# Performance work log

Hardware: AMD Instinct MI355X
Metric: run time of the kernel (lower is better)

## Reference

```python
import jax, jax.numpy as jnp
import numpy as np

_J6 = jnp.array([[0,0,0,0,0,1],[0,0,0,0,-1,0],[0,0,0,1,0,0],[0,0,1,0,0,0],[0,-1,0,0,0,0],[1,0,0,0,0,0]], dtype=jnp.float32)
# pairs (i,j) from combinations(range(4),2)
_PI = jnp.array([0,0,0,1,1,2])
_PJ = jnp.array([1,2,3,2,3,3])

def exterior(p1, p2):
    # p1, p2: [B,T,H,4] -> Plucker line coords [B,T,H,6], L2-normalized
    L = p1[..., _PI] * p2[..., _PJ] - p1[..., _PJ] * p2[..., _PI]
    n = jnp.clip(jnp.linalg.norm(L, axis=-1, keepdims=True), 1e-12)
    return L / n

def setup_inputs() -> dict:
    key = jax.random.key(0)
    ks = jax.random.split(key, 8)
    B, T, D, H = 2, 2048, 1024, 16
    pd = 4
    s = 0.02
    return {
        "x": jax.random.normal(ks[0], (B, T, D), jnp.float32),
        "w_qkv": jax.random.normal(ks[1], (3 * D, D), jnp.float32) * s,
        "b_qkv": jnp.zeros((3 * D,), jnp.float32),
        "w1_write": jax.random.normal(ks[2], (pd * H, D), jnp.float32) * s,
        "w2_write": jax.random.normal(ks[3], (pd * H, D), jnp.float32) * s,
        "w1_read": jax.random.normal(ks[4], (pd * H, D), jnp.float32) * s,
        "w2_read": jax.random.normal(ks[5], (pd * H, D), jnp.float32) * s,
        "w_out": jax.random.normal(ks[6], (D, D), jnp.float32) * s,
        "b_out": jnp.zeros((D,), jnp.float32),
        "decay_logits": jnp.full((H,), 4.6, jnp.float32),
        "bias_scale": jnp.full((H,), 0.1, jnp.float32),
    }

def reference(x, w_qkv, b_qkv, w1_write, w2_write, w1_read, w2_read, w_out, b_out, decay_logits, bias_scale):
    B, T, D = x.shape
    H = decay_logits.shape[0]
    dh = D // H
    pd = w1_write.shape[0] // H
    scale = dh ** -0.5

    qkv = (x @ w_qkv.T + b_qkv).reshape(B, T, 3, H, dh)
    qkv = jnp.transpose(qkv, (2, 0, 3, 1, 4))  # [3,B,H,T,dh]
    q, k, v = qkv[0], qkv[1], qkv[2]
    std_logits = jnp.einsum('bhqd,bhkd->bhqk', q, k) * scale

    x_prev = jnp.concatenate([jnp.zeros((B, 1, D), x.dtype), x[:, :-1]], axis=1)
    w1 = (x_prev @ w1_write.T).reshape(B, T, H, pd)
    w2 = (x @ w2_write.T).reshape(B, T, H, pd)
    write_lines = exterior(w1, w2)  # [B,T,H,6]
    r1 = (x @ w1_read.T).reshape(B, T, H, pd)
    r2 = (x @ w2_read.T).reshape(B, T, H, pd)
    read_lines = exterior(r1, r2)

    J_write = jnp.einsum('bthi,ij->bthj', write_lines, _J6)
    incidence = jnp.einsum('bqhp,bkhp->bhqk', read_lines, J_write)  # [B,H,T,T]

    decays = jax.nn.sigmoid(decay_logits)  # [H]
    pos = jnp.arange(T, dtype=x.dtype)
    diffs = pos[:, None] - pos[None, :]  # [T,T], q - k
    past = diffs > 0
    diffs_pos = jnp.where(past, diffs, 0.0)
    weights = (decays[:, None, None] ** diffs_pos[None]) * past[None].astype(x.dtype)  # [H,T,T]

    bias = incidence * weights[None] * bias_scale[None, :, None, None]
    logits = std_logits + bias
    causal_mask = diffs < 0  # k > q -> masked
    logits = jnp.where(causal_mask[None, None], -jnp.inf, logits)
    attn = jax.nn.softmax(logits, axis=-1)
    out = jnp.einsum('bhqk,bhkd->bqhd', attn, v).reshape(B, T, D)
    return out @ w_out.T + b_out
```

## Files before the change

### kernel.cpp

```cpp
#include <hip/hip_runtime.h>
#include <hip/hip_bf16.h>

using bhalf = __hip_bfloat16;
typedef __bf16 bf16x8 __attribute__((ext_vector_type(8)));
typedef __bf16 bf16x2 __attribute__((ext_vector_type(2)));
typedef float f32x4 __attribute__((ext_vector_type(4)));

#define B_DIM 2
#define T_DIM 2048
#define D_DIM 1024
#define H_DIM 16
#define DH 64

struct bh8 { bhalf v[8]; };
struct bh4 { bhalf v[4]; };

__device__ __forceinline__ bf16x8 load_bf16x8(const bhalf* p) {
    return __builtin_bit_cast(bf16x8, *(const uint4*)p);
}
__device__ __forceinline__ bf16x8 zero_bf16x8() {
    uint4 z; z.x = 0; z.y = 0; z.z = 0; z.w = 0;
    return __builtin_bit_cast(bf16x8, z);
}
__device__ __forceinline__ void stage8_cvt(bhalf* dst, const float* src) {
    float4 a = *(const float4*)src;
    float4 b = *(const float4*)(src + 4);
    bh8 t;
    t.v[0] = __float2bfloat16(a.x); t.v[1] = __float2bfloat16(a.y);
    t.v[2] = __float2bfloat16(a.z); t.v[3] = __float2bfloat16(a.w);
    t.v[4] = __float2bfloat16(b.x); t.v[5] = __float2bfloat16(b.y);
    t.v[6] = __float2bfloat16(b.z); t.v[7] = __float2bfloat16(b.w);
    *(uint4*)dst = __builtin_bit_cast(uint4, t);
}

#define GLD16(gp, lp) __builtin_amdgcn_global_load_lds( \
    (const __attribute__((address_space(1))) void*)(gp), \
    (__attribute__((address_space(3))) void*)(lp), 16, 0, 0)

#define SX  4194304
#define SW  3145728
#define SL  65536
#define SO  1048576
__global__ __launch_bounds__(256) void cvt_all(
    const float* __restrict__ x, const float* __restrict__ wqkv,
    const float* __restrict__ w1w, const float* __restrict__ w2w,
    const float* __restrict__ w1r, const float* __restrict__ w2r,
    const float* __restrict__ wout,
    bhalf* __restrict__ xbf, bhalf* __restrict__ wcat, bhalf* __restrict__ woutbf)
{
    int i = (blockIdx.x * 256 + threadIdx.x) * 8;
    if (i < SX) { stage8_cvt(xbf + i, x + i); return; }
    i -= SX;
    if (i < SW) { stage8_cvt(wcat + i, wqkv + i); return; }
    i -= SW;
    if (i < SL) { stage8_cvt(wcat + SW + i, w1w + i); return; }
    i -= SL;
    if (i < SL) { stage8_cvt(wcat + SW + SL + i, w2w + i); return; }
    i -= SL;
    if (i < SL) { stage8_cvt(wcat + SW + 2 * SL + i, w1r + i); return; }
    i -= SL;
    if (i < SL) { stage8_cvt(wcat + SW + 3 * SL + i, w2r + i); return; }
    i -= SL;
    if (i < SO) { stage8_cvt(woutbf + i, wout + i); }
}

__device__ __forceinline__ void gemm128_mainloop(
    const bhalf* __restrict__ A, const bhalf* __restrict__ B, int K,
    bhalf* As, bhalf* Bs, f32x4 acc[4][4])
{
    const int tid = threadIdx.x;
    const int wave = tid >> 6, lane = tid & 63;
    const int ln = lane & 15, lg = lane >> 4;
    const int wr = (wave >> 1) * 64, wc = (wave & 1) * 64;
    const int lrow = lane >> 3;
    const int lcol = (lane & 7) * 8;

    for (int kt = 0; kt < K; kt += 64) {
        __syncthreads();
#pragma unroll
        for (int i = 0; i < 4; ++i) {
            int idx = __builtin_amdgcn_readfirstlane(wave * 4 + i);
            GLD16(A + (size_t)(idx * 8 + lrow) * K + kt + lcol, As + idx * 512);
            GLD16(B + (size_t)(idx * 8 + lrow) * K + kt + lcol, Bs + idx * 512);
        }
        __syncthreads();
#pragma unroll
        for (int ks = 0; ks < 2; ++ks) {
            bf16x8 af[4], bfr[4];
#pragma unroll
            for (int mt = 0; mt < 4; ++mt)
                af[mt] = load_bf16x8(As + (wr + mt * 16 + ln) * 64 + ks * 32 + lg * 8);
#pragma unroll
            for (int nt = 0; nt < 4; ++nt)
                bfr[nt] = load_bf16x8(Bs + (wc + nt * 16 + ln) * 64 + ks * 32 + lg * 8);
#pragma unroll
            for (int mt = 0; mt < 4; ++mt)
#pragma unroll
                for (int nt = 0; nt < 4; ++nt)
                    acc[mt][nt] = __builtin_amdgcn_mfma_f32_16x16x32_bf16(af[mt], bfr[nt], acc[mt][nt], 0, 0, 0);
        }
    }
}

__global__ __launch_bounds__(256) void qkv_lines_gemm128(
    const bhalf* __restrict__ x, const bhalf* __restrict__ wcat, const float* __restrict__ bqkv,
    bhalf* __restrict__ qo, bhalf* __restrict__ ko, bhalf* __restrict__ vt,
    float* __restrict__ proj)
{
    __shared__ bhalf As[128 * 64];
    __shared__ bhalf Bs[128 * 64];
    f32x4 acc[4][4] = {};
    gemm128_mainloop(x + (size_t)blockIdx.x * 128 * D_DIM,
                     wcat + (size_t)blockIdx.y * 128 * D_DIM, D_DIM, As, Bs, acc);
    const int wave = threadIdx.x >> 6, lane = threadIdx.x & 63;
    const int ln = lane & 15, lg = lane >> 4;
    const int wr = (wave >> 1) * 64, wc = (wave & 1) * 64;
    const int trip = (blockIdx.y * 128) >> 10;

    if (trip == 2) {
#pragma unroll
        for (int nt = 0; nt < 4; ++nt) {
            int n = blockIdx.y * 128 + wc + nt * 16 + ln;
            float bias = bqkv[n];
            int h = (n >> 6) & 15, d = n & 63;
#pragma unroll
            for (int mt = 0; mt < 4; ++mt) {
                int tok0 = blockIdx.x * 128 + wr + mt * 16 + lg * 4;
                int b = tok0 >> 11, t0 = tok0 & (T_DIM - 1);
                bh4 pk;
#pragma unroll
                for (int r = 0; r < 4; ++r)
                    pk.v[r] = __float2bfloat16(acc[mt][nt][r] + bias);
                *(uint2*)&vt[(((size_t)(b * H_DIM + h)) * DH + d) * T_DIM + t0] =
                    __builtin_bit_cast(uint2, pk);
            }
        }
    } else {
#pragma unroll
        for (int nt = 0; nt < 4; ++nt) {
            int n = blockIdx.y * 128 + wc + nt * 16 + ln;
            int h = (n >> 6) & 15, d = n & 63;
            float bias = (trip < 3) ? bqkv[n] : 0.f;
#pragma unroll
            for (int mt = 0; mt < 4; ++mt)
#pragma unroll
                for (int r = 0; r < 4; ++r) {
                    int tok = blockIdx.x * 128 + wr + mt * 16 + lg * 4 + r;
                    int b = tok >> 11, t = tok & (T_DIM - 1);
                    float y = acc[mt][nt][r] + bias;
                    if (trip == 0) {
                        qo[(((size_t)(b * H_DIM + h)) * T_DIM + t) * DH + d] = __float2bfloat16(y * 0.18033688f);
                    } else if (trip == 1) {
                        ko[(((size_t)(b * H_DIM + h)) * T_DIM + t) * DH + d] = __float2bfloat16(y);
                    } else {
                        proj[(size_t)tok * 256 + (n - 3072)] = y;
                    }
                }
        }
    }
}

__global__ __launch_bounds__(256) void out_gemm64(
    const bhalf* __restrict__ a, const bhalf* __restrict__ w, const float* __restrict__ bo,
    float* __restrict__ out)
{
    __shared__ bhalf As[64 * 64];
    __shared__ bhalf Bs[64 * 64];
    const int tid = threadIdx.x;
    const int wave = tid >> 6, lane = tid & 63;
    const int ln = lane & 15, lg = lane >> 4;
    const int lrow = lane >> 3;
    const int lcol = (lane & 7) * 8;
    const bhalf* A = a + (size_t)blockIdx.x * 64 * D_DIM;
    const bhalf* B = w + (size_t)blockIdx.y * 64 * D_DIM;
    f32x4 acc[4] = {};

    for (int kt = 0; kt < D_DIM; kt += 64) {
        __syncthreads();
#pragma unroll
        for (int i = 0; i < 2; ++i) {
            int idx = __builtin_amdgcn_readfirstlane(wave * 2 + i);
            GLD16(A + (size_t)(idx * 8 + lrow) * D_DIM + kt + lcol, As + idx * 512);
            GLD16(B + (size_t)(idx * 8 + lrow) * D_DIM + kt + lcol, Bs + idx * 512);
        }
        __syncthreads();
#pragma unroll
        for (int ks = 0; ks < 2; ++ks) {
            bf16x8 af = load_bf16x8(As + (wave * 16 + ln) * 64 + ks * 32 + lg * 8);
#pragma unroll
            for (int nt = 0; nt < 4; ++nt) {
                bf16x8 bfr = load_bf16x8(Bs + (nt * 16 + ln) * 64 + ks * 32 + lg * 8);
                acc[nt] = __builtin_amdgcn_mfma_f32_16x16x32_bf16(af, bfr, acc[nt], 0, 0, 0);
            }
        }
    }
#pragma unroll
    for (int nt = 0; nt < 4; ++nt) {
        int n = blockIdx.y * 64 + nt * 16 + ln;
        float bias = bo[n];
#pragma unroll
        for (int r = 0; r < 4; ++r) {
            int tok = blockIdx.x * 64 + wave * 16 + lg * 4 + r;
            out[(size_t)tok * D_DIM + n] = acc[nt][r] + bias;
        }
    }
}

__global__ __launch_bounds__(256) void build_lines(
    const float* __restrict__ proj, const float* __restrict__ bias_scale,
    const float* __restrict__ decay_logits,
    bhalf* __restrict__ read8, bhalf* __restrict__ jw8)
{
    int id = blockIdx.x * 256 + threadIdx.x;
    int tok = id >> 4, h = id & 15;
    int b = tok >> 11, t = tok & (T_DIM - 1);
    const float* pr = proj + (size_t)tok * 256;

    float p1[4], p2[4], r1[4], r2[4];
#pragma unroll
    for (int i = 0; i < 4; ++i) {
        p1[i] = (t > 0) ? pr[-256 + h * 4 + i] : 0.f;
        p2[i] = pr[64 + h * 4 + i];
        r1[i] = pr[128 + h * 4 + i];
        r2[i] = pr[192 + h * 4 + i];
    }
    float Lw[6], Lr[6];
    {
        Lw[0] = p1[0] * p2[1] - p1[1] * p2[0];
        Lw[1] = p1[0] * p2[2] - p1[2] * p2[0];
        Lw[2] = p1[0] * p2[3] - p1[3] * p2[0];
        Lw[3] = p1[1] * p2[2] - p1[2] * p2[1];
        Lw[4] = p1[1] * p2[3] - p1[3] * p2[1];
        Lw[5] = p1[2] * p2[3] - p1[3] * p2[2];
        float n2 = 0.f;
#pragma unroll
        for (int j = 0; j < 6; ++j) n2 += Lw[j] * Lw[j];
        float inv = 1.f / fmaxf(sqrtf(n2), 1e-12f);
#pragma unroll
        for (int j = 0; j < 6; ++j) Lw[j] *= inv;
    }
    {
        Lr[0] = r1[0] * r2[1] - r1[1] * r2[0];
        Lr[1] = r1[0] * r2[2] - r1[2] * r2[0];
        Lr[2] = r1[0] * r2[3] - r1[3] * r2[0];
        Lr[3] = r1[1] * r2[2] - r1[2] * r2[1];
        Lr[4] = r1[1] * r2[3] - r1[3] * r2[1];
        Lr[5] = r1[2] * r2[3] - r1[3] * r2[2];
        float n2 = 0.f;
#pragma unroll
        for (int j = 0; j < 6; ++j) n2 += Lr[j] * Lr[j];
        float inv = 1.f / fmaxf(sqrtf(n2), 1e-12f);
#pragma unroll
        for (int j = 0; j < 6; ++j) Lr[j] *= inv;
    }
    float decay = 1.f / (1.f + __expf(-decay_logits[h]));
    float l2d = log2f(decay);
    float bs = bias_scale[h] * exp2f(-(float)t * l2d);
    size_t base = (((size_t)(b * H_DIM + h)) * T_DIM + t) * 8;
    read8[base + 0] = __float2bfloat16(Lr[0]);
    read8[base + 1] = __float2bfloat16(Lr[1]);
    read8[base + 2] = __float2bfloat16(Lr[2]);
    read8[base + 3] = __float2bfloat16(Lr[3]);
    read8[base + 4] = __float2bfloat16(Lr[4]);
    read8[base + 5] = __float2bfloat16(Lr[5]);
    read8[base + 6] = __float2bfloat16(0.f);
    read8[base + 7] = __float2bfloat16(0.f);
    jw8[base + 0] = __float2bfloat16(Lw[5] * bs);
    jw8[base + 1] = __float2bfloat16(-Lw[4] * bs);
    jw8[base + 2] = __float2bfloat16(Lw[3] * bs);
    jw8[base + 3] = __float2bfloat16(Lw[2] * bs);
    jw8[base + 4] = __float2bfloat16(-Lw[1] * bs);
    jw8[base + 5] = __float2bfloat16(Lw[0] * bs);
    jw8[base + 6] = __float2bfloat16(0.f);
    jw8[base + 7] = __float2bfloat16(0.f);
}

template<bool DIAG>
__device__ __forceinline__ void tile_step(
    const f32x4& z0, const f32x4& z1, const f32x4& i0, const f32x4& i1,
    int rq, int kb, const float* aq, int lg, int ln, bhalf* pl, float* lp)
{
#pragma unroll
    for (int r = 0; r < 4; ++r) {
        float p0, p1;
        if (DIAG) {
            int diff0 = rq + lg * 4 + r - (kb + 2 * ln);
            float s0 = z0[r] + ((diff0 > 0) ? i0[r] * aq[r] : 0.f);
            p0 = (diff0 < 0) ? 0.f : __builtin_amdgcn_exp2f(s0);
            int diff1 = diff0 - 1;
            float s1 = z1[r] + ((diff1 > 0) ? i1[r] * aq[r] : 0.f);
            p1 = (diff1 < 0) ? 0.f : __builtin_amdgcn_exp2f(s1);
        } else {
            p0 = __builtin_amdgcn_exp2f(fmaf(i0[r], aq[r], z0[r]));
            p1 = __builtin_amdgcn_exp2f(fmaf(i1[r], aq[r], z1[r]));
        }
        bf16x2 h2;
        h2.x = (__bf16)p0;
        h2.y = (__bf16)p1;
        *(unsigned int*)&pl[(lg * 4 + r) * 72 + 2 * ln] = __builtin_bit_cast(unsigned int, h2);
        lp[r] += p0 + p1;
    }
}

#define MFMA_BF16 __builtin_amdgcn_mfma_f32_16x16x32_bf16

#define QKSM64(T) { \
    { f32x4 z0 = {}, z1 = {}, i0 = {}, i1 = {}; \
      z0 = MFMA_BF16(q##T##0, k00, z0, 0, 0, 0); \
      z0 = MFMA_BF16(q##T##1, k01, z0, 0, 0, 0); \
      i0 = MFMA_BF16(rf##T, j0, i0, 0, 0, 0); \
      z1 = MFMA_BF16(q##T##0, k10, z1, 0, 0, 0); \
      z1 = MFMA_BF16(q##T##1, k11, z1, 0, 0, 0); \
      i1 = MFMA_BF16(rf##T, j1, i1, 0, 0, 0); \
      if (c == nc##T - 1 && (t##T & 3) < 2) \
          tile_step<true >(z0, z1, i0, i1, rq##T, kb, aq##T, lg, ln, pl##T, lp##T); \
      else \
          tile_step<false>(z0, z1, i0, i1, rq##T, kb, aq##T, lg, ln, pl##T, lp##T); \
    } \
    { f32x4 z0 = {}, z1 = {}, i0 = {}, i1 = {}; \
      z0 = MFMA_BF16(q##T##0, k00b, z0, 0, 0, 0); \
      z0 = MFMA_BF16(q##T##1, k01b, z0, 0, 0, 0); \
      i0 = MFMA_BF16(rf##T, j0b, i0, 0, 0, 0); \
      z1 = MFMA_BF16(q##T##0, k10b, z1, 0, 0, 0); \
      z1 = MFMA_BF16(q##T##1, k11b, z1, 0, 0, 0); \
      i1 = MFMA_BF16(rf##T, j1b, i1, 0, 0, 0); \
      if (c == nc##T - 1) \
          tile_step<true >(z0, z1, i0, i1, rq##T, kb + 32, aq##T, lg, ln, pl##T + 32, lp##T); \
      else \
          tile_step<false>(z0, z1, i0, i1, rq##T, kb + 32, aq##T, lg, ln, pl##T + 32, lp##T); \
    } }

#define PVSTEP64(T) { \
    bf16x8 pf0 = load_bf16x8(pl##T + ln * 72 + lg * 8); \
    bf16x8 pf1 = load_bf16x8(pl##T + ln * 72 + 32 + lg * 8); \
    o##T[0] = MFMA_BF16(pf0, vf0, o##T[0], 0, 0, 0); \
    o##T[1] = MFMA_BF16(pf0, vf1, o##T[1], 0, 0, 0); \
    o##T[2] = MFMA_BF16(pf0, vf2, o##T[2], 0, 0, 0); \
    o##T[3] = MFMA_BF16(pf0, vf3, o##T[3], 0, 0, 0); \
    o##T[0] = MFMA_BF16(pf1, vf4, o##T[0], 0, 0, 0); \
    o##T[1] = MFMA_BF16(pf1, vf5, o##T[1], 0, 0, 0); \
    o##T[2] = MFMA_BF16(pf1, vf6, o##T[2], 0, 0, 0); \
    o##T[3] = MFMA_BF16(pf1, vf7, o##T[3], 0, 0, 0); }

#define WRITE_OUT(T) { \
    __syncthreads(); \
    _Pragma("unroll") \
    for (int r = 0; r < 4; ++r) { \
        if (ln == 0) sm[wave * 1088 + (lg * 4 + r) * 68 + 64] = lp##T[r]; \
        _Pragma("unroll") \
        for (int nt = 0; nt < 4; ++nt) \
            sm[wave * 1088 + (lg * 4 + r) * 68 + nt * 16 + ln] = o##T[nt][r]; \
    } \
    __syncthreads(); \
    { \
        float l = 0.f; \
        _Pragma("unroll") \
        for (int w = 0; w < 4; ++w) l += sm[w * 1088 + row * 68 + 64]; \
        float4 acc = {0.f, 0.f, 0.f, 0.f}; \
        _Pragma("unroll") \
        for (int w = 0; w < 4; ++w) { \
            float4 t = *(const float4*)&sm[w * 1088 + row * 68 + c4]; \
            acc.x += t.x; acc.y += t.y; acc.z += t.z; acc.w += t.w; \
        } \
        float invl = 1.f / l; \
        bh4 pk; \
        pk.v[0] = __float2bfloat16(acc.x * invl); \
        pk.v[1] = __float2bfloat16(acc.y * invl); \
        pk.v[2] = __float2bfloat16(acc.z * invl); \
        pk.v[3] = __float2bfloat16(acc.w * invl); \
        size_t tok = (size_t)b * T_DIM + rq##T + row; \
        *(uint2*)&attn_out[tok * D_DIM + h * DH + c4] = __builtin_bit_cast(uint2, pk); \
    } }

__global__ __launch_bounds__(256) void attn_kernel(
    const bhalf* __restrict__ q, const bhalf* __restrict__ k, const bhalf* __restrict__ vt,
    const bhalf* __restrict__ read8, const bhalf* __restrict__ jw8,
    const float* __restrict__ decay_logits, bhalf* __restrict__ attn_out)
{
    __shared__ float sm[9216];
    const int wave = threadIdx.x >> 6, lane = threadIdx.x & 63;
    const int ln = lane & 15, lg = lane >> 4;
    const int bx = blockIdx.x;
    const int xcd = bx & 7;
    const int slot = bx >> 3;
    const int hbid = xcd * 4 + (slot >> 5);
    const int h = hbid & 15, b = hbid >> 4;
    const int j = slot & 31;
    const int tA = j, tB = 63 - j, tC = 64 + j, tD = 127 - j;
    const int rqA = tA * 16, rqB = tB * 16, rqC = tC * 16, rqD = tD * 16;
    const int ncA = (tA >> 2) + 1, ncB = (tB >> 2) + 1;
    const int ncC = (tC >> 2) + 1, ncD = (tD >> 2) + 1;
    const size_t hb = (size_t)(b * H_DIM + h);
    const bhalf* qh = q + hb * T_DIM * DH;
    const bhalf* kh = k + hb * T_DIM * DH;
    const bhalf* vh = vt + hb * DH * T_DIM;
    const bhalf* r8 = read8 + hb * T_DIM * 8;
    const bhalf* j8 = jw8 + hb * T_DIM * 8;

    bhalf* plA = (bhalf*)sm + 0 * 4608 + wave * 1152;
    bhalf* plB = (bhalf*)sm + 1 * 4608 + wave * 1152;
    bhalf* plC = (bhalf*)sm + 2 * 4608 + wave * 1152;
    bhalf* plD = (bhalf*)sm + 3 * 4608 + wave * 1152;

    bf16x8 zf = zero_bf16x8();
    bf16x8 qA0 = load_bf16x8(qh + (rqA + ln) * DH + lg * 8);
    bf16x8 qA1 = load_bf16x8(qh + (rqA + ln) * DH + 32 + lg * 8);
    bf16x8 qB0 = load_bf16x8(qh + (rqB + ln) * DH + lg * 8);
    bf16x8 qB1 = load_bf16x8(qh + (rqB + ln) * DH + 32 + lg * 8);
    bf16x8 qC0 = load_bf16x8(qh + (rqC + ln) * DH + lg * 8);
    bf16x8 qC1 = load_bf16x8(qh + (rqC + ln) * DH + 32 + lg * 8);
    bf16x8 qD0 = load_bf16x8(qh + (rqD + ln) * DH + lg * 8);
    bf16x8 qD1 = load_bf16x8(qh + (rqD + ln) * DH + 32 + lg * 8);
    bf16x8 rfA = (lane < 16) ? load_bf16x8(r8 + (size_t)(rqA + ln) * 8) : zf;
    bf16x8 rfB = (lane < 16) ? load_bf16x8(r8 + (size_t)(rqB + ln) * 8) : zf;
    bf16x8 rfC = (lane < 16) ? load_bf16x8(r8 + (size_t)(rqC + ln) * 8) : zf;
    bf16x8 rfD = (lane < 16) ? load_bf16x8(r8 + (size_t)(rqD + ln) * 8) : zf;

    float decay = 1.f / (1.f + __expf(-decay_logits[h]));
    float l2d = log2f(decay);
    const float LOG2E = 1.44269504f;
    float aqA[4], aqB[4], aqC[4], aqD[4];
#pragma unroll
    for (int r = 0; r < 4; ++r) {
        aqA[r] = LOG2E * __builtin_amdgcn_exp2f((float)(rqA + lg * 4 + r) * l2d);
        aqB[r] = LOG2E * __builtin_amdgcn_exp2f((float)(rqB + lg * 4 + r) * l2d);
        aqC[r] = LOG2E * __builtin_amdgcn_exp2f((float)(rqC + lg * 4 + r) * l2d);
        aqD[r] = LOG2E * __builtin_amdgcn_exp2f((float)(rqD + lg * 4 + r) * l2d);
    }

    f32x4 oA[4] = {}, oB[4] = {}, oC[4] = {}, oD[4] = {};
    float lpA[4] = {}, lpB[4] = {}, lpC[4] = {}, lpD[4] = {};

    for (int c = wave; c < ncD; c += 4) {
        const int kb = c * 64;
        bf16x8 k00 = load_bf16x8(kh + (kb + 2 * ln) * DH + lg * 8);
        bf16x8 k01 = load_bf16x8(kh + (kb + 2 * ln) * DH + 32 + lg * 8);
        bf16x8 k10 = load_bf16x8(kh + (kb + 2 * ln + 1) * DH + lg * 8);
        bf16x8 k11 = load_bf16x8(kh + (kb + 2 * ln + 1) * DH + 32 + lg * 8);
        bf16x8 j0 = (lane < 16) ? load_bf16x8(j8 + (size_t)(kb + 2 * ln) * 8) : zf;
        bf16x8 j1 = (lane < 16) ? load_bf16x8(j8 + (size_t)(kb + 2 * ln + 1) * 8) : zf;
        bf16x8 k00b = load_bf16x8(kh + (kb + 32 + 2 * ln) * DH + lg * 8);
        bf16x8 k01b = load_bf16x8(kh + (kb + 32 + 2 * ln) * DH + 32 + lg * 8);
        bf16x8 k10b = load_bf16x8(kh + (kb + 32 + 2 * ln + 1) * DH + lg * 8);
        bf16x8 k11b = load_bf16x8(kh + (kb + 32 + 2 * ln + 1) * DH + 32 + lg * 8);
        bf16x8 j0b = (lane < 16) ? load_bf16x8(j8 + (size_t)(kb + 32 + 2 * ln) * 8) : zf;
        bf16x8 j1b = (lane < 16) ? load_bf16x8(j8 + (size_t)(kb + 32 + 2 * ln + 1) * 8) : zf;
        bf16x8 vf0 = load_bf16x8(vh + (size_t)(ln) * T_DIM + kb + lg * 8);
        bf16x8 vf1 = load_bf16x8(vh + (size_t)(16 + ln) * T_DIM + kb + lg * 8);
        bf16x8 vf2 = load_bf16x8(vh + (size_t)(32 + ln) * T_DIM + kb + lg * 8);
        bf16x8 vf3 = load_bf16x8(vh + (size_t)(48 + ln) * T_DIM + kb + lg * 8);
        bf16x8 vf4 = load_bf16x8(vh + (size_t)(ln) * T_DIM + kb + 32 + lg * 8);
        bf16x8 vf5 = load_bf16x8(vh + (size_t)(16 + ln) * T_DIM + kb + 32 + lg * 8);
        bf16x8 vf6 = load_bf16x8(vh + (size_t)(32 + ln) * T_DIM + kb + 32 + lg * 8);
        bf16x8 vf7 = load_bf16x8(vh + (size_t)(48 + ln) * T_DIM + kb + 32 + lg * 8);
        const bool doC = (c < ncC), doB = (c < ncB), doA = (c < ncA);

        QKSM64(D);
        if (doC) QKSM64(C);
        if (doB) QKSM64(B);
        if (doA) QKSM64(A);

        PVSTEP64(D);
        if (doC) PVSTEP64(C);
        if (doB) PVSTEP64(B);
        if (doA) PVSTEP64(A);
    }

#pragma unroll
    for (int r = 0; r < 4; ++r) {
#pragma unroll
        for (int off = 1; off < 16; off <<= 1) {
            lpA[r] += __shfl_xor(lpA[r], off, 16);
            lpB[r] += __shfl_xor(lpB[r], off, 16);
            lpC[r] += __shfl_xor(lpC[r], off, 16);
            lpD[r] += __shfl_xor(lpD[r], off, 16);
        }
    }

    const int row = threadIdx.x >> 4;
    const int c4 = (threadIdx.x & 15) * 4;

    WRITE_OUT(A);
    WRITE_OUT(B);
    WRITE_OUT(C);
    WRITE_OUT(D);
}

extern "C" void kernel_launch(void* const* d_in, const int* in_sizes, int n_in,
                              void* d_out, int out_size, void* d_ws, size_t ws_size,
                              hipStream_t stream)
{
    const float* x    = (const float*)d_in[0];
    const float* wqkv = (const float*)d_in[1];
    const float* bqkv = (const float*)d_in[2];
    const float* w1w  = (const float*)d_in[3];
    const float* w2w  = (const float*)d_in[4];
    const float* w1r  = (const float*)d_in[5];
    const float* w2r  = (const float*)d_in[6];
    const float* wout = (const float*)d_in[7];
    const float* bout = (const float*)d_in[8];
    const float* dlog = (const float*)d_in[9];
    const float* bsc  = (const float*)d_in[10];
    float* out = (float*)d_out;

    char* ws = (char*)d_ws;
    bhalf* qb    = (bhalf*)(ws);
    bhalf* kbuf  = (bhalf*)(ws + 8388608);
    bhalf* vtb   = (bhalf*)(ws + 16777216);
    bhalf* r8    = (bhalf*)(ws + 25165824);
    bhalf* j8    = (bhalf*)(ws + 26214400);
    float* proj  = (float*)(ws + 27262976);
    bhalf* ao    = (bhalf*)(ws + 31457280);
    bhalf* woutbf = (bhalf*)(ws + 39845888);

    bhalf* xbf  = (bhalf*)d_out;
    bhalf* wcat = (bhalf*)((char*)d_out + 8388608);

    cvt_all<<<4224, 256, 0, stream>>>(x, wqkv, w1w, w2w, w1r, w2r, wout, xbf, wcat, woutbf);
    qkv_lines_gemm128<<<dim3(32, 26), 256, 0, stream>>>(xbf, wcat, bqkv, qb, kbuf, vtb, proj);
    build_lines<<<256, 256, 0, stream>>>(proj, bsc, dlog, r8, j8);
    attn_kernel<<<1024, 256, 0, stream>>>(qb, kbuf, vtb, r8, j8, dlog, ao);
    out_gemm64<<<dim3(64, 16), 256, 0, stream>>>(ao, woutbf, bout, out);
}
```

Measured before the change: 258.1 us.

## Compute transposed QK^T so P fragments stay in registers for PV MFMA

Swaps MFMA operand order so the score tile comes out transposed (keys along rows per lane), which matches the A-operand layout needed by the PV MFMA. The probability fragments are packed directly into bf16x8 registers instead of being written to LDS and read back, removing the LDS round trip and shrinking shared memory. Row-sum bookkeeping becomes a single scalar per lane with a cheaper cross-lane reduction. It adds register pressure from holding eight P fragments per iteration.

```diff
diff --git a/kernel.cpp b/kernel.cpp
--- a/kernel.cpp
+++ b/kernel.cpp
@@ -276,77 +276,78 @@
 }
 
 template<bool DIAG>
-__device__ __forceinline__ void tile_step(
-    const f32x4& z0, const f32x4& z1, const f32x4& i0, const f32x4& i1,
-    int rq, int kb, const float* aq, int lg, int ln, bhalf* pl, float* lp)
-{
+__device__ __forceinline__ bf16x8 tile_step_sw(
+    const f32x4& ze, const f32x4& zo, const f32x4& ie, const f32x4& io,
+    int qrow, int kb, int lg, float aq, float& lp)
+{
+    bf16x8 pf;
+    float s = lp;
 #pragma unroll
     for (int r = 0; r < 4; ++r) {
-        float p0, p1;
+        float pe, po;
         if (DIAG) {
-            int diff0 = rq + lg * 4 + r - (kb + 2 * ln);
-            float s0 = z0[r] + ((diff0 > 0) ? i0[r] * aq[r] : 0.f);
-            p0 = (diff0 < 0) ? 0.f : __builtin_amdgcn_exp2f(s0);
-            int diff1 = diff0 - 1;
-            float s1 = z1[r] + ((diff1 > 0) ? i1[r] * aq[r] : 0.f);
-            p1 = (diff1 < 0) ? 0.f : __builtin_amdgcn_exp2f(s1);
+            int de = qrow - (kb + 8 * lg + 2 * r);
+            float se = ze[r] + ((de > 0) ? ie[r] * aq : 0.f);
+            pe = (de < 0) ? 0.f : __builtin_amdgcn_exp2f(se);
+            int dd = de - 1;
+            float so = zo[r] + ((dd > 0) ? io[r] * aq : 0.f);
+            po = (dd < 0) ? 0.f : __builtin_amdgcn_exp2f(so);
         } else {
-            p0 = __builtin_amdgcn_exp2f(fmaf(i0[r], aq[r], z0[r]));
-            p1 = __builtin_amdgcn_exp2f(fmaf(i1[r], aq[r], z1[r]));
-        }
-        bf16x2 h2;
-        h2.x = (__bf16)p0;
-        h2.y = (__bf16)p1;
-        *(unsigned int*)&pl[(lg * 4 + r) * 72 + 2 * ln] = __builtin_bit_cast(unsigned int, h2);
-        lp[r] += p0 + p1;
-    }
+            pe = __builtin_amdgcn_exp2f(fmaf(ie[r], aq, ze[r]));
+            po = __builtin_amdgcn_exp2f(fmaf(io[r], aq, zo[r]));
+        }
+        pf[2 * r]     = (__bf16)pe;
+        pf[2 * r + 1] = (__bf16)po;
+        s += pe + po;
+    }
+    lp = s;
+    return pf;
 }
 
 #define MFMA_BF16 __builtin_amdgcn_mfma_f32_16x16x32_bf16
 
 #define QKSM64(T) { \
-    { f32x4 z0 = {}, z1 = {}, i0 = {}, i1 = {}; \
-      z0 = MFMA_BF16(q##T##0, k00, z0, 0, 0, 0); \
-      z0 = MFMA_BF16(q##T##1, k01, z0, 0, 0, 0); \
-      i0 = MFMA_BF16(rf##T, j0, i0, 0, 0, 0); \
-      z1 = MFMA_BF16(q##T##0, k10, z1, 0, 0, 0); \
-      z1 = MFMA_BF16(q##T##1, k11, z1, 0, 0, 0); \
-      i1 = MFMA_BF16(rf##T, j1, i1, 0, 0, 0); \
-      if (c == nc##T - 1 && (t##T & 3) < 2) \
-          tile_step<true >(z0, z1, i0, i1, rq##T, kb, aq##T, lg, ln, pl##T, lp##T); \
+    const bool last##T = (c == nc##T - 1); \
+    { f32x4 ze = {}, zo = {}, ie = {}, io = {}; \
+      ze = MFMA_BF16(k00, q##T##0, ze, 0, 0, 0); \
+      ze = MFMA_BF16(k01, q##T##1, ze, 0, 0, 0); \
+      zo = MFMA_BF16(k10, q##T##0, zo, 0, 0, 0); \
+      zo = MFMA_BF16(k11, q##T##1, zo, 0, 0, 0); \
+      ie = MFMA_BF16(j0, rf##T, ie, 0, 0, 0); \
+      io = MFMA_BF16(j1, rf##T, io, 0, 0, 0); \
+      if (last##T && (t##T & 3) < 2) \
+          pfa##T = tile_step_sw<true >(ze, zo, ie, io, qr##T, kb, lg, aq##T, lp##T); \
       else \
-          tile_step<false>(z0, z1, i0, i1, rq##T, kb, aq##T, lg, ln, pl##T, lp##T); \
+          pfa##T = tile_step_sw<false>(ze, zo, ie, io, qr##T, kb, lg, aq##T, lp##T); \
     } \
-    { f32x4 z0 = {}, z1 = {}, i0 = {}, i1 = {}; \
-      z0 = MFMA_BF16(q##T##0, k00b, z0, 0, 0, 0); \
-      z0 = MFMA_BF16(q##T##1, k01b, z0, 0, 0, 0); \
-      i0 = MFMA_BF16(rf##T, j0b, i0, 0, 0, 0); \
-      z1 = MFMA_BF16(q##T##0, k10b, z1, 0, 0, 0); \
-      z1 = MFMA_BF16(q##T##1, k11b, z1, 0, 0, 0); \
-      i1 = MFMA_BF16(rf##T, j1b, i1, 0, 0, 0); \
-      if (c == nc##T - 1) \
-          tile_step<true >(z0, z1, i0, i1, rq##T, kb + 32, aq##T, lg, ln, pl##T + 32, lp##T); \
+    { f32x4 ze = {}, zo = {}, ie = {}, io = {}; \
+      ze = MFMA_BF16(k00b, q##T##0, ze, 0, 0, 0); \
+      ze = MFMA_BF16(k01b, q##T##1, ze, 0, 0, 0); \
+      zo = MFMA_BF16(k10b, q##T##0, zo, 0, 0, 0); \
+      zo = MFMA_BF16(k11b, q##T##1, zo, 0, 0, 0); \
+      ie = MFMA_BF16(j0b, rf##T, ie, 0, 0, 0); \
+      io = MFMA_BF16(j1b, rf##T, io, 0, 0, 0); \
+      if (last##T) \
+          pfb##T = tile_step_sw<true >(ze, zo, ie, io, qr##T, kb + 32, lg, aq##T, lp##T); \
       else \
-          tile_step<false>(z0, z1, i0, i1, rq##T, kb + 32, aq##T, lg, ln, pl##T + 32, lp##T); \
+          pfb##T = tile_step_sw<false>(ze, zo, ie, io, qr##T, kb + 32, lg, aq##T, lp##T); \
     } }
 
 #define PVSTEP64(T) { \
-    bf16x8 pf0 = load_bf16x8(pl##T + ln * 72 + lg * 8); \
-    bf16x8 pf1 = load_bf16x8(pl##T + ln * 72 + 32 + lg * 8); \
-    o##T[0] = MFMA_BF16(pf0, vf0, o##T[0], 0, 0, 0); \
-    o##T[1] = MFMA_BF16(pf0, vf1, o##T[1], 0, 0, 0); \
-    o##T[2] = MFMA_BF16(pf0, vf2, o##T[2], 0, 0, 0); \
-    o##T[3] = MFMA_BF16(pf0, vf3, o##T[3], 0, 0, 0); \
-    o##T[0] = MFMA_BF16(pf1, vf4, o##T[0], 0, 0, 0); \
-    o##T[1] = MFMA_BF16(pf1, vf5, o##T[1], 0, 0, 0); \
-    o##T[2] = MFMA_BF16(pf1, vf6, o##T[2], 0, 0, 0); \
-    o##T[3] = MFMA_BF16(pf1, vf7, o##T[3], 0, 0, 0); }
+    o##T[0] = MFMA_BF16(pfa##T, vf0, o##T[0], 0, 0, 0); \
+    o##T[1] = MFMA_BF16(pfa##T, vf1, o##T[1], 0, 0, 0); \
+    o##T[2] = MFMA_BF16(pfa##T, vf2, o##T[2], 0, 0, 0); \
+    o##T[3] = MFMA_BF16(pfa##T, vf3, o##T[3], 0, 0, 0); \
+    o##T[0] = MFMA_BF16(pfb##T, vf4, o##T[0], 0, 0, 0); \
+    o##T[1] = MFMA_BF16(pfb##T, vf5, o##T[1], 0, 0, 0); \
+    o##T[2] = MFMA_BF16(pfb##T, vf6, o##T[2], 0, 0, 0); \
+    o##T[3] = MFMA_BF16(pfb##T, vf7, o##T[3], 0, 0, 0); }
 
 #define WRITE_OUT(T) { \
     __syncthreads(); \
+    if (lg == 0) sm[wave * 1088 + ln * 68 + 64] = lp##T; \
     _Pragma("unroll") \
     for (int r = 0; r < 4; ++r) { \
-        if (ln == 0) sm[wave * 1088 + (lg * 4 + r) * 68 + 64] = lp##T[r]; \
         _Pragma("unroll") \
         for (int nt = 0; nt < 4; ++nt) \
             sm[wave * 1088 + (lg * 4 + r) * 68 + nt * 16 + ln] = o##T[nt][r]; \
@@ -377,7 +378,7 @@
     const bhalf* __restrict__ read8, const bhalf* __restrict__ jw8,
     const float* __restrict__ decay_logits, bhalf* __restrict__ attn_out)
 {
-    __shared__ float sm[9216];
+    __shared__ float sm[4352];
     const int wave = threadIdx.x >> 6, lane = threadIdx.x & 63;
     const int ln = lane & 15, lg = lane >> 4;
     const int bx = blockIdx.x;
@@ -390,17 +391,13 @@
     const int rqA = tA * 16, rqB = tB * 16, rqC = tC * 16, rqD = tD * 16;
     const int ncA = (tA >> 2) + 1, ncB = (tB >> 2) + 1;
     const int ncC = (tC >> 2) + 1, ncD = (tD >> 2) + 1;
+    const int qrA = rqA + ln, qrB = rqB + ln, qrC = rqC + ln, qrD = rqD + ln;
     const size_t hb = (size_t)(b * H_DIM + h);
     const bhalf* qh = q + hb * T_DIM * DH;
     const bhalf* kh = k + hb * T_DIM * DH;
     const bhalf* vh = vt + hb * DH * T_DIM;
     const bhalf* r8 = read8 + hb * T_DIM * 8;
     const bhalf* j8 = jw8 + hb * T_DIM * 8;
-
-    bhalf* plA = (bhalf*)sm + 0 * 4608 + wave * 1152;
-    bhalf* plB = (bhalf*)sm + 1 * 4608 + wave * 1152;
-    bhalf* plC = (bhalf*)sm + 2 * 4608 + wave * 1152;
-    bhalf* plD = (bhalf*)sm + 3 * 4608 + wave * 1152;
 
     bf16x8 zf = zero_bf16x8();
     bf16x8 qA0 = load_bf16x8(qh + (rqA + ln) * DH + lg * 8);
@@ -419,17 +416,13 @@
     float decay = 1.f / (1.f + __expf(-decay_logits[h]));
     float l2d = log2f(decay);
     const float LOG2E = 1.44269504f;
-    float aqA[4], aqB[4], aqC[4], aqD[4];
-#pragma unroll
-    for (int r = 0; r < 4; ++r) {
-        aqA[r] = LOG2E * __builtin_amdgcn_exp2f((float)(rqA + lg * 4 + r) * l2d);
-        aqB[r] = LOG2E * __builtin_amdgcn_exp2f((float)(rqB + lg * 4 + r) * l2d);
-        aqC[r] = LOG2E * __builtin_amdgcn_exp2f((float)(rqC + lg * 4 + r) * l2d);
-        aqD[r] = LOG2E * __builtin_amdgcn_exp2f((float)(rqD + lg * 4 + r) * l2d);
-    }
+    float aqA = LOG2E * __builtin_amdgcn_exp2f((float)qrA * l2d);
+    float aqB = LOG2E * __builtin_amdgcn_exp2f((float)qrB * l2d);
+    float aqC = LOG2E * __builtin_amdgcn_exp2f((float)qrC * l2d);
+    float aqD = LOG2E * __builtin_amdgcn_exp2f((float)qrD * l2d);
 
     f32x4 oA[4] = {}, oB[4] = {}, oC[4] = {}, oD[4] = {};
-    float lpA[4] = {}, lpB[4] = {}, lpC[4] = {}, lpD[4] = {};
+    float lpA = 0.f, lpB = 0.f, lpC = 0.f, lpD = 0.f;
 
     for (int c = wave; c < ncD; c += 4) {
         const int kb = c * 64;
@@ -455,6 +448,7 @@
         bf16x8 vf7 = load_bf16x8(vh + (size_t)(48 + ln) * T_DIM + kb + 32 + lg * 8);
         const bool doC = (c < ncC), doB = (c < ncB), doA = (c < ncA);
 
+        bf16x8 pfaD, pfbD, pfaC, pfbC, pfaB, pfbB, pfaA, pfbA;
         QKSM64(D);
         if (doC) QKSM64(C);
         if (doB) QKSM64(B);
@@ -466,16 +460,10 @@
         if (doA) PVSTEP64(A);
     }
 
-#pragma unroll
-    for (int r = 0; r < 4; ++r) {
-#pragma unroll
-        for (int off = 1; off < 16; off <<= 1) {
-            lpA[r] += __shfl_xor(lpA[r], off, 16);
-            lpB[r] += __shfl_xor(lpB[r], off, 16);
-            lpC[r] += __shfl_xor(lpC[r], off, 16);
-            lpD[r] += __shfl_xor(lpD[r], off, 16);
-        }
-    }
+    lpA += __shfl_xor(lpA, 16); lpA += __shfl_xor(lpA, 32);
+    lpB += __shfl_xor(lpB, 16); lpB += __shfl_xor(lpB, 32);
+    lpC += __shfl_xor(lpC, 16); lpC += __shfl_xor(lpC, 32);
+    lpD += __shfl_xor(lpD, 16); lpD += __shfl_xor(lpD, 32);
 
     const int row = threadIdx.x >> 4;
     const int c4 = (threadIdx.x & 15) * 4;
```

After: 256.6 us. About the same (-0.6%).
